# Kernel tuning notes

Measured on AMD Instinct MI355X. Metric: run time of the kernel, lower is better.

Reference implementation:

```python
import jax, jax.numpy as jnp
import numpy as np

T, K, F = 131072, 64, 8
EPS = 1e-10


def setup_inputs() -> dict:
    key = jax.random.key(0)
    k0, k1, k2, k3 = jax.random.split(key, 4)
    return {
        "observations": jax.random.normal(k0, (T, F), dtype=jnp.float32),
        "beta_logits": jax.random.normal(k1, (K,), dtype=jnp.float32),
        "pi_logits": jax.random.normal(k2, (K, K), dtype=jnp.float32),
        "means": 0.1 * jax.random.normal(k3, (K, F), dtype=jnp.float32),
        "log_vars": jnp.zeros((K, F), dtype=jnp.float32),
    }


def _stick_breaking(logits):
    betas = jax.nn.sigmoid(logits)
    cp = jnp.cumprod(1.0 - betas)
    return betas * jnp.concatenate([jnp.ones((1,), betas.dtype), cp[:-1]])


def _emission_log_probs(obs, means, log_vars):
    # Diagonal-covariance MVN log-prob, vectorized over (T, K) via matmuls
    # logN(x; mu, diag(v)) = -0.5 * (sum((x-mu)^2/v) + sum(log v) + F*log(2pi))
    inv_var = jnp.exp(-log_vars)                                 # (K, F)
    quad = (obs ** 2) @ inv_var.T                                # (T, K): sum x^2/v
    cross = obs @ (means * inv_var).T                            # (T, K): sum x*mu/v
    const = jnp.sum(means ** 2 * inv_var + log_vars, axis=1)     # (K,)
    log2pi = jnp.float32(np.log(2.0 * np.pi))
    Fdim = obs.shape[1]
    return -0.5 * (quad - 2.0 * cross + const[None, :] + Fdim * log2pi)


def reference(observations, beta_logits, pi_logits, means, log_vars):
    beta_w = _stick_breaking(beta_logits)                        # (K,)
    trans = jax.nn.softmax(pi_logits, axis=1)                    # (K, K)
    em = jnp.exp(_emission_log_probs(observations, means, log_vars))  # (T, K)

    # Forward recursion
    a0 = beta_w * em[0]
    a0 = a0 / (a0.sum() + EPS)

    def fwd_step(a, e):
        a = (a @ trans) * e
        a = a / (a.sum() + EPS)
        return a, a

    _, alpha_rest = jax.lax.scan(fwd_step, a0, em[1:])
    alpha = jnp.concatenate([a0[None, :], alpha_rest], axis=0)   # (T, K)

    # Backward recursion: beta[t] = normalize(trans @ (beta[t+1] * em[t+1]))
    bT = jnp.ones((trans.shape[0],), observations.dtype)

    def bwd_step(b, e_next):
        b = trans @ (b * e_next)
        b = b / (b.sum() + EPS)
        return b, b

    _, beta_rev = jax.lax.scan(bwd_step, bT, em[1:], reverse=True)
    beta = jnp.concatenate([beta_rev, bT[None, :]], axis=0)      # (T, K)

    log_likelihood = jnp.log(alpha[-1].sum() + EPS)
    return alpha, beta, log_likelihood
```

## Files before the change

### kernel.cpp

```cpp
#include <hip/hip_runtime.h>

#define T_N   131072
#define K_N   64
#define L_C   128
#define F_N   8
#define N_CH  (T_N / L_C)
#define WARM  96
#define EPS_F 1e-10f
#define OBS_MAX ((T_N - 1) * F_N)

#define LOG2E 1.4426950408889634f
#define NL2E  (-0.72134752044448170f)
#define LN2   0.6931471805599453f
#define LN2PI 1.8378770664093453f

typedef float v2f __attribute__((ext_vector_type(2)));

__device__ __forceinline__ float dpp_f(float x, const int ctrl) {
  return x;
}
#define DPPI(SRC, CTRL) __builtin_amdgcn_update_dpp(0, (SRC), (CTRL), 0xF, 0xF, true)
#define DPPF(SRC, CTRL) __int_as_float(DPPI(__float_as_int(SRC), (CTRL)))

template <int CTRL>
__device__ __forceinline__ float dpp_add(float x) {
  int y = __builtin_amdgcn_update_dpp(0, __float_as_int(x), CTRL, 0xF, 0xF, true);
  return x + __int_as_float(y);
}
__device__ __forceinline__ float wave_sum64(float x) {
  x = dpp_add<0x111>(x);
  x = dpp_add<0x112>(x);
  x = dpp_add<0x114>(x);
  x = dpp_add<0x118>(x);
  x = dpp_add<0x142>(x);
  x = dpp_add<0x143>(x);
  return __int_as_float(__builtin_amdgcn_readlane(__float_as_int(x), 63));
}

#define PKFMA(a, b, c) __builtin_elementwise_fma(a, b, c)

__device__ __forceinline__ float em_pk(const float4& xa, const float4& xb,
                                       const v2f civ2[4], const v2f cmiv2[4],
                                       float ccst) {
  v2f x0 = {xa.x, xa.y}, x1 = {xa.z, xa.w};
  v2f x2 = {xb.x, xb.y}, x3 = {xb.z, xb.w};
  v2f a0 = {ccst, 0.f}, a1 = {0.f, 0.f};
  a0 = PKFMA(x0, PKFMA(x0, civ2[0], cmiv2[0]), a0);
  a1 = PKFMA(x1, PKFMA(x1, civ2[1], cmiv2[1]), a1);
  a0 = PKFMA(x2, PKFMA(x2, civ2[2], cmiv2[2]), a0);
  a1 = PKFMA(x3, PKFMA(x3, civ2[3], cmiv2[3]), a1);
  v2f s = a0 + a1;
  return __builtin_amdgcn_exp2f(s.x + s.y);
}

#define MATVEC(VV, MOUT)                                                      \
  {                                                                           \
    float Gr[16];                                                             \
    Gr[0] = (VV);                                                             \
    Gr[1] = DPPF(Gr[0], 0xB1);                                 \
    Gr[2] = DPPF(Gr[0], 0x4E);                                 \
    Gr[3] = DPPF(Gr[1], 0x4E);                                                \
    _Pragma("unroll")                                                         \
    for (int rr = 0; rr < 4; ++rr) Gr[4 + rr] = DPPF(Gr[rr], 0x124);          \
    _Pragma("unroll")                                                         \
    for (int rr = 0; rr < 8; ++rr) Gr[8 + rr] = DPPF(Gr[rr], 0x128);          \
    v2f aE0 = {0.f,0.f}, aE1 = {0.f,0.f}, aO0 = {0.f,0.f}, aO1 = {0.f,0.f};   \
    _Pragma("unroll")                                                         \
    for (int rr = 0; rr < 8; ++rr) {                                          \
      v2f gg = {Gr[rr], Gr[rr]};                                              \
      aE0 = PKFMA(gg, TcE[rr], aE0);                                          \
      aO0 = PKFMA(gg, TcO[rr], aO0);                                          \
    }                                                                         \
    _Pragma("unroll")                                                         \
    for (int rr = 8; rr < 16; ++rr) {                                         \
      v2f gg = {Gr[rr], Gr[rr]};                                              \
      aE1 = PKFMA(gg, TcE[rr], aE1);                                          \
      aO1 = PKFMA(gg, TcO[rr], aO1);                                          \
    }                                                                         \
    v2f accE = aE0 + aE1, accO = aO0 + aO1;           \
    float kx = qb0 ? accO.x : accE.x, ky = qb0 ? accO.y : accE.y;             \
    float sx = qb0 ? accE.x : accO.x, sy = qb0 ? accE.y : accO.y;             \
    float rx = __int_as_float(                                                \
        __builtin_amdgcn_ds_swizzle(__float_as_int(sx), 0x401F));             \
    float ry = __int_as_float(                                                \
        __builtin_amdgcn_ds_swizzle(__float_as_int(sy), 0x401F));             \
    float c0 = kx + rx, c1 = ky + ry;                 \
    float keep2 = qb1 ? c1 : c0;                                              \
    float send2 = qb1 ? c0 : c1;                                              \
    float got = __int_as_float(                                               \
        __builtin_amdgcn_ds_bpermute(bpaddr, __float_as_int(send2)));         \
    MOUT = keep2 + got;                             \
  }

extern "C" __global__ void __launch_bounds__(64, 2)
hdphmm_fb(const float* __restrict__ obs,
          const float* __restrict__ beta_logits,
          const float* __restrict__ pi_logits,
          const float* __restrict__ means,
          const float* __restrict__ log_vars,
          float* __restrict__ out) {
  const int lane = threadIdx.x;
  const int bid  = blockIdx.x;
  const int h    = lane & 15;
  const int q    = lane >> 4;
  const bool qb0 = (q & 1);
  const bool qb1 = (q >> 1);
  const int bpaddr = (lane ^ 32) << 2;
  __shared__ __align__(8) float2 sstat[K_N];
  __shared__ float sb[K_N];

  float* alpha   = out;
  float* betaout = out + (size_t)T_N * K_N;

  v2f civ2[4], cmiv2[4];
  float ccst;
  {
    const float4* mp = reinterpret_cast<const float4*>(means + lane * F_N);
    const float4* lp = reinterpret_cast<const float4*>(log_vars + lane * F_N);
    float4 m0 = mp[0], m1 = mp[1];
    float4 l0 = lp[0], l1 = lp[1];
    float mu[8] = {m0.x, m0.y, m0.z, m0.w, m1.x, m1.y, m1.z, m1.w};
    float lv[8] = {l0.x, l0.y, l0.z, l0.w, l1.x, l1.y, l1.z, l1.w};
    float cst = F_N * LN2PI;
#pragma unroll
    for (int f = 0; f < 8; ++f) {
      float iv = __builtin_amdgcn_exp2f(-lv[f] * LOG2E);
      cst += lv[f] + mu[f] * mu[f] * iv;
      float cf  = NL2E * iv;
      civ2[f >> 1][f & 1]  = cf;
      cmiv2[f >> 1][f & 1] = -2.0f * mu[f] * cf;
    }
    ccst = NL2E * cst;
  }

  {
    const float4* pr4 = reinterpret_cast<const float4*>(pi_logits + lane * K_N);
    float mx = -3.0e38f;
#pragma unroll
    for (int k = 0; k < 16; ++k) {
      float4 r = pr4[k];
      mx = fmaxf(mx, fmaxf(fmaxf(r.x, r.y), fmaxf(r.z, r.w)));
    }
    float s = 0.0f;
#pragma unroll
    for (int k = 0; k < 16; ++k) {
      float4 r = pr4[k];
      s += __builtin_amdgcn_exp2f((r.x - mx) * LOG2E);
      s += __builtin_amdgcn_exp2f((r.y - mx) * LOG2E);
      s += __builtin_amdgcn_exp2f((r.z - mx) * LOG2E);
      s += __builtin_amdgcn_exp2f((r.w - mx) * LOG2E);
    }
    sstat[lane] = make_float2(mx, __builtin_amdgcn_rcpf(s));
  }
  __syncthreads();

  int ki[16];
  ki[0] = lane;
  ki[1] = DPPI(ki[0], 0xB1);
  ki[2] = DPPI(ki[0], 0x4E);
  ki[3] = DPPI(ki[1], 0x4E);
#pragma unroll
  for (int rr = 0; rr < 4; ++rr) ki[4 + rr] = DPPI(ki[rr], 0x124);
#pragma unroll
  for (int rr = 0; rr < 8; ++rr) ki[8 + rr] = DPPI(ki[rr], 0x128);

  if (bid < N_CH) {
    v2f TcE[16], TcO[16];
#pragma unroll
    for (int rr = 0; rr < 16; ++rr) {
      int k = ki[rr];
      float2 st = sstat[k];
      const float* pk = pi_logits + k * K_N;
      float e0 = __builtin_amdgcn_exp2f((pk[h]      - st.x) * LOG2E) * st.y;
      float e1 = __builtin_amdgcn_exp2f((pk[h + 16] - st.x) * LOG2E) * st.y;
      float e2 = __builtin_amdgcn_exp2f((pk[h + 32] - st.x) * LOG2E) * st.y;
      float e3 = __builtin_amdgcn_exp2f((pk[h + 48] - st.x) * LOG2E) * st.y;
      TcE[rr] = (v2f){e0, e2};
      TcO[rr] = (v2f){e1, e3};
    }

    const int out_lo = bid * L_C;
    float v;
    int t_first;
    if (bid == 0) {
      float bl = beta_logits[lane];
      float ex = __builtin_amdgcn_exp2f(-bl * LOG2E);
      float bw = __builtin_amdgcn_rcpf(1.0f + ex);
      sb[lane] = 1.0f - bw;
      __syncthreads();
      float pr = 1.0f;
#pragma unroll
      for (int i = 0; i < 64; ++i) {
        float qv = sb[i];
        pr = (i < lane) ? pr * qv : pr;
      }
      float4 x0 = reinterpret_cast<const float4*>(obs)[0];
      float4 x1 = reinterpret_cast<const float4*>(obs)[1];
      v = bw * pr * em_pk(x0, x1, civ2, cmiv2, ccst);
      t_first = 1;
    } else {
      const int t0 = out_lo - WARM;
      const float4* xp = reinterpret_cast<const float4*>(obs + t0 * F_N);
      v = em_pk(xp[0], xp[1], civ2, cmiv2, ccst);
      t_first = t0 + 1;
    }
    float S = wave_sum64(v);
    int obs_off = t_first * F_N;
    float4 xa, xb;
    {
      const float4* xp = reinterpret_cast<const float4*>(obs + obs_off);
      xa = xp[0]; xb = xp[1];
    }
    int out_off = out_lo * K_N + lane;

#define FWD_STEP(DO_STORE)                                                    \
  {                                                                           \
    int offn = obs_off + F_N; offn = (offn > OBS_MAX) ? OBS_MAX : offn;       \
    float4 nxa = *reinterpret_cast<const float4*>(obs + offn);                \
    float4 nxb = *reinterpret_cast<const float4*>(obs + offn + 4);            \
    float m;                                                                  \
    MATVEC(v, m)                                                              \
    float r = __builtin_amdgcn_rcpf(S + EPS_F);                               \
    if (DO_STORE) { alpha[out_off] = v * r; out_off += K_N; }                 \
    float e = em_pk(xa, xb, civ2, cmiv2, ccst);                               \
    float vn = m * r * e;                                                     \
    S = wave_sum64(vn);                                                       \
    v = vn; xa = nxa; xb = nxb; obs_off = offn;                               \
  }

    const int wn = (bid == 0) ? 0 : WARM;
#pragma unroll 1
    for (int it = 0; it < wn; ++it) FWD_STEP(0)
#pragma unroll 1
    for (int it = 0; it < L_C - 1; ++it) FWD_STEP(1)
#undef FWD_STEP
    float r = __builtin_amdgcn_rcpf(S + EPS_F);
    alpha[out_off] = v * r;
    if (bid == N_CH - 1 && lane == 0) {
      float sl = S * r + EPS_F;
      out[(size_t)2 * T_N * K_N] = __builtin_amdgcn_logf(sl) * LN2;
    }
  } else {
    v2f TcE[16], TcO[16];
    {
      float2 s0 = sstat[h], s1 = sstat[h + 16];
      float2 s2 = sstat[h + 32], s3 = sstat[h + 48];
#pragma unroll
      for (int rr = 0; rr < 16; ++rr) {
        int k = ki[rr];
        float p0 = pi_logits[h * K_N + k];
        float p1 = pi_logits[(h + 16) * K_N + k];
        float p2 = pi_logits[(h + 32) * K_N + k];
        float p3 = pi_logits[(h + 48) * K_N + k];
        TcE[rr] = (v2f){__builtin_amdgcn_exp2f((p0 - s0.x) * LOG2E) * s0.y,
                        __builtin_amdgcn_exp2f((p2 - s2.x) * LOG2E) * s2.y};
        TcO[rr] = (v2f){__builtin_amdgcn_exp2f((p1 - s1.x) * LOG2E) * s1.y,
                        __builtin_amdgcn_exp2f((p3 - s3.x) * LOG2E) * s3.y};
      }
    }
    const int cb   = bid - N_CH;
    const int t_lo = cb * L_C;
    const int t_hi = t_lo + L_C - 1;
    int t_top = t_hi + WARM;
    if (t_top > T_N - 1) t_top = T_N - 1;
    const int s_top = (cb == N_CH - 1) ? T_N - 2 : t_hi;

    float u = 1.0f, S = 1.0f;
    float w;
    {
      const float4* xp = reinterpret_cast<const float4*>(obs + t_top * F_N);
      w = em_pk(xp[0], xp[1], civ2, cmiv2, ccst);
    }
    if (cb == N_CH - 1)
      betaout[(size_t)(T_N - 1) * K_N + lane] = 1.0f;
    int obs_off = (t_top - 1) * F_N;
    float4 xa, xb;
    {
      const float4* xp = reinterpret_cast<const float4*>(obs + obs_off);
      xa = xp[0]; xb = xp[1];
    }
    int out_off = s_top * K_N + lane;

#define BWD_STEP(DO_STORE)                                                    \
  {                                                                           \
    int offn = obs_off - F_N; offn = (offn < 0) ? 0 : offn;                   \
    float4 nxa = *reinterpret_cast<const float4*>(obs + offn);                \
    float4 nxb = *reinterpret_cast<const float4*>(obs + offn + 4);            \
    float m;                                                                  \
    MATVEC(w, m)                                                              \
    float r = __builtin_amdgcn_rcpf(S + EPS_F);                               \
    if (DO_STORE) { betaout[out_off] = u * r; out_off -= K_N; }               \
    float u2 = m * r;                                                         \
    float e = em_pk(xa, xb, civ2, cmiv2, ccst);                               \
    w = u2 * e;                                                               \
    S = wave_sum64(u2);                                                       \
    u = u2; xa = nxa; xb = nxb; obs_off = offn;                               \
  }

    const int warm_n  = t_top - s_top;
    const int store_n = s_top - t_lo;
#pragma unroll 1
    for (int it = 0; it < warm_n; ++it) BWD_STEP(0)
#pragma unroll 1
    for (int it = 0; it < store_n; ++it) BWD_STEP(1)
#undef BWD_STEP
    betaout[t_lo * K_N + lane] = u * __builtin_amdgcn_rcpf(S + EPS_F);
  }
}

extern "C" void kernel_launch(void* const* d_in, const int* in_sizes, int n_in,
                              void* d_out, int out_size, void* d_ws, size_t ws_size,
                              hipStream_t stream) {
  (void)in_sizes; (void)n_in; (void)out_size; (void)d_ws; (void)ws_size;
  const float* obs  = (const float*)d_in[0];
  const float* bl   = (const float*)d_in[1];
  const float* pi   = (const float*)d_in[2];
  const float* mns  = (const float*)d_in[3];
  const float* lvs  = (const float*)d_in[4];
  hipLaunchKernelGGL(hdphmm_fb, dim3(2 * N_CH), dim3(64), 0, stream,
                     obs, bl, pi, mns, lvs, (float*)d_out);
}
```

Before: 181.2 us.

## Batch warm-up normalisation every eight steps and use permlane swaps in matvec

During the warm-up phase of both the forward and backward chunked recursions, the per-step wave reduction and reciprocal are replaced by a renormalisation every eight steps. Emissions are scaled by a constant exponent offset so values stay in range between renormalisations. The matvec cross-quadrant reduction now uses permlane16/32 swap builtins where available, replacing ds_swizzle and ds_bpermute. The storing loops compute the reciprocal one step ahead and are unrolled by two. The intent is to shorten the serial critical path per step, at the cost of more reliance on the fixed scale offset to avoid overflow or underflow.

```diff
diff --git a/kernel.cpp b/kernel.cpp
--- a/kernel.cpp
+++ b/kernel.cpp
@@ -13,12 +13,11 @@
 #define NL2E  (-0.72134752044448170f)
 #define LN2   0.6931471805599453f
 #define LN2PI 1.8378770664093453f
+#define EMSC  16.0f
 
 typedef float v2f __attribute__((ext_vector_type(2)));
-
-__device__ __forceinline__ float dpp_f(float x, const int ctrl) {
-  return x;
-}
+typedef unsigned uint2v __attribute__((ext_vector_type(2)));
+
 #define DPPI(SRC, CTRL) __builtin_amdgcn_update_dpp(0, (SRC), (CTRL), 0xF, 0xF, true)
 #define DPPF(SRC, CTRL) __int_as_float(DPPI(__float_as_int(SRC), (CTRL)))
 
@@ -37,14 +36,38 @@
   return __int_as_float(__builtin_amdgcn_readlane(__float_as_int(x), 63));
 }
 
+#if __has_builtin(__builtin_amdgcn_permlane16_swap) && \
+    __has_builtin(__builtin_amdgcn_permlane32_swap)
+__device__ __forceinline__ float psum16(float x) {
+  uint2v r = __builtin_amdgcn_permlane16_swap(__float_as_uint(x),
+                                              __float_as_uint(x), false, false);
+  return __uint_as_float(r.x) + __uint_as_float(r.y);
+}
+__device__ __forceinline__ float psum32(float x) {
+  uint2v r = __builtin_amdgcn_permlane32_swap(__float_as_uint(x),
+                                              __float_as_uint(x), false, false);
+  return __uint_as_float(r.x) + __uint_as_float(r.y);
+}
+#else
+__device__ __forceinline__ float psum16(float x) {
+  return x + __int_as_float(
+      __builtin_amdgcn_ds_swizzle(__float_as_int(x), 0x401F));
+}
+__device__ __forceinline__ float psum32(float x) {
+  int addr = (((int)threadIdx.x ^ 32) & 63) << 2;
+  return x + __int_as_float(
+      __builtin_amdgcn_ds_bpermute(addr, __float_as_int(x)));
+}
+#endif
+
 #define PKFMA(a, b, c) __builtin_elementwise_fma(a, b, c)
 
 __device__ __forceinline__ float em_pk(const float4& xa, const float4& xb,
                                        const v2f civ2[4], const v2f cmiv2[4],
-                                       float ccst) {
+                                       float cc) {
   v2f x0 = {xa.x, xa.y}, x1 = {xa.z, xa.w};
   v2f x2 = {xb.x, xb.y}, x3 = {xb.z, xb.w};
-  v2f a0 = {ccst, 0.f}, a1 = {0.f, 0.f};
+  v2f a0 = {cc, 0.f}, a1 = {0.f, 0.f};
   a0 = PKFMA(x0, PKFMA(x0, civ2[0], cmiv2[0]), a0);
   a1 = PKFMA(x1, PKFMA(x1, civ2[1], cmiv2[1]), a1);
   a0 = PKFMA(x2, PKFMA(x2, civ2[2], cmiv2[2]), a0);
@@ -78,18 +101,13 @@
       aO1 = PKFMA(gg, TcO[rr], aO1);                                          \
     }                                                                         \
     v2f accE = aE0 + aE1, accO = aO0 + aO1;           \
-    float kx = qb0 ? accO.x : accE.x, ky = qb0 ? accO.y : accE.y;             \
-    float sx = qb0 ? accE.x : accO.x, sy = qb0 ? accE.y : accO.y;             \
-    float rx = __int_as_float(                                                \
-        __builtin_amdgcn_ds_swizzle(__float_as_int(sx), 0x401F));             \
-    float ry = __int_as_float(                                                \
-        __builtin_amdgcn_ds_swizzle(__float_as_int(sy), 0x401F));             \
-    float c0 = kx + rx, c1 = ky + ry;                 \
-    float keep2 = qb1 ? c1 : c0;                                              \
-    float send2 = qb1 ? c0 : c1;                                              \
-    float got = __int_as_float(                                               \
-        __builtin_amdgcn_ds_bpermute(bpaddr, __float_as_int(send2)));         \
-    MOUT = keep2 + got;                             \
+    float pe0 = psum32(accE.x), pe2 = psum32(accE.y);                         \
+    float po1 = psum32(accO.x), po3 = psum32(accO.y);                         \
+    pe0 = psum16(pe0); pe2 = psum16(pe2);                                     \
+    po1 = psum16(po1); po3 = psum16(po3);                                     \
+    float tE = qb1 ? pe2 : pe0;                                               \
+    float tO = qb1 ? po3 : po1;                                               \
+    MOUT = qb0 ? tO : tE;                                                     \
   }
 
 extern "C" __global__ void __launch_bounds__(64, 2)
@@ -102,10 +120,8 @@
   const int lane = threadIdx.x;
   const int bid  = blockIdx.x;
   const int h    = lane & 15;
-  const int q    = lane >> 4;
-  const bool qb0 = (q & 1);
-  const bool qb1 = (q >> 1);
-  const int bpaddr = (lane ^ 32) << 2;
+  const bool qb0 = (lane >> 4) & 1;
+  const bool qb1 = (lane >> 5) & 1;
   __shared__ __align__(8) float2 sstat[K_N];
   __shared__ float sb[K_N];
 
@@ -113,7 +129,7 @@
   float* betaout = out + (size_t)T_N * K_N;
 
   v2f civ2[4], cmiv2[4];
-  float ccst;
+  float c0, cw;
   {
     const float4* mp = reinterpret_cast<const float4*>(means + lane * F_N);
     const float4* lp = reinterpret_cast<const float4*>(log_vars + lane * F_N);
@@ -130,7 +146,8 @@
       civ2[f >> 1][f & 1]  = cf;
       cmiv2[f >> 1][f & 1] = -2.0f * mu[f] * cf;
     }
-    ccst = NL2E * cst;
+    c0 = NL2E * cst;
+    cw = c0 + EMSC;
   }
 
   {
@@ -196,15 +213,14 @@
       }
       float4 x0 = reinterpret_cast<const float4*>(obs)[0];
       float4 x1 = reinterpret_cast<const float4*>(obs)[1];
-      v = bw * pr * em_pk(x0, x1, civ2, cmiv2, ccst);
+      v = bw * pr * em_pk(x0, x1, civ2, cmiv2, c0);
       t_first = 1;
     } else {
       const int t0 = out_lo - WARM;
       const float4* xp = reinterpret_cast<const float4*>(obs + t0 * F_N);
-      v = em_pk(xp[0], xp[1], civ2, cmiv2, ccst);
+      v = em_pk(xp[0], xp[1], civ2, cmiv2, cw);
       t_first = t0 + 1;
     }
-    float S = wave_sum64(v);
     int obs_off = t_first * F_N;
     float4 xa, xb;
     {
@@ -213,31 +229,47 @@
     }
     int out_off = out_lo * K_N + lane;
 
-#define FWD_STEP(DO_STORE)                                                    \
+    const int wn8 = (bid == 0) ? 0 : (WARM >> 3);
+#pragma unroll 1
+    for (int o = 0; o < wn8; ++o) {
+#pragma unroll
+      for (int i = 0; i < 8; ++i) {
+        float4 nxa = *reinterpret_cast<const float4*>(obs + obs_off + F_N);
+        float4 nxb = *reinterpret_cast<const float4*>(obs + obs_off + F_N + 4);
+        float m;
+        MATVEC(v, m)
+        float e = em_pk(xa, xb, civ2, cmiv2, cw);
+        v = m * e;
+        xa = nxa; xb = nxb; obs_off += F_N;
+      }
+      float Sw = wave_sum64(v);
+      v *= __builtin_amdgcn_rcpf(Sw);
+    }
+
+    float S = wave_sum64(v);
+    float r_st = __builtin_amdgcn_rcpf(S + EPS_F);
+
+#define FWD_SSTEP                                                             \
   {                                                                           \
     int offn = obs_off + F_N; offn = (offn > OBS_MAX) ? OBS_MAX : offn;       \
     float4 nxa = *reinterpret_cast<const float4*>(obs + offn);                \
     float4 nxb = *reinterpret_cast<const float4*>(obs + offn + 4);            \
     float m;                                                                  \
     MATVEC(v, m)                                                              \
-    float r = __builtin_amdgcn_rcpf(S + EPS_F);                               \
-    if (DO_STORE) { alpha[out_off] = v * r; out_off += K_N; }                 \
-    float e = em_pk(xa, xb, civ2, cmiv2, ccst);                               \
-    float vn = m * r * e;                                                     \
+    alpha[out_off] = v * r_st; out_off += K_N;                                \
+    float e = em_pk(xa, xb, civ2, cmiv2, c0);                                 \
+    float vn = m * (r_st * e);                                                \
     S = wave_sum64(vn);                                                       \
+    r_st = __builtin_amdgcn_rcpf(S + EPS_F);                                  \
     v = vn; xa = nxa; xb = nxb; obs_off = offn;                               \
   }
 
-    const int wn = (bid == 0) ? 0 : WARM;
-#pragma unroll 1
-    for (int it = 0; it < wn; ++it) FWD_STEP(0)
-#pragma unroll 1
-    for (int it = 0; it < L_C - 1; ++it) FWD_STEP(1)
-#undef FWD_STEP
-    float r = __builtin_amdgcn_rcpf(S + EPS_F);
-    alpha[out_off] = v * r;
+#pragma unroll 2
+    for (int it = 0; it < L_C - 1; ++it) FWD_SSTEP
+#undef FWD_SSTEP
+    alpha[out_off] = v * r_st;
     if (bid == N_CH - 1 && lane == 0) {
-      float sl = S * r + EPS_F;
+      float sl = S * r_st + EPS_F;
       out[(size_t)2 * T_N * K_N] = __builtin_amdgcn_logf(sl) * LN2;
     }
   } else {
@@ -265,11 +297,10 @@
     if (t_top > T_N - 1) t_top = T_N - 1;
     const int s_top = (cb == N_CH - 1) ? T_N - 2 : t_hi;
 
-    float u = 1.0f, S = 1.0f;
     float w;
     {
       const float4* xp = reinterpret_cast<const float4*>(obs + t_top * F_N);
-      w = em_pk(xp[0], xp[1], civ2, cmiv2, ccst);
+      w = em_pk(xp[0], xp[1], civ2, cmiv2, cw);
     }
     if (cb == N_CH - 1)
       betaout[(size_t)(T_N - 1) * K_N + lane] = 1.0f;
@@ -281,30 +312,67 @@
     }
     int out_off = s_top * K_N + lane;
 
-#define BWD_STEP(DO_STORE)                                                    \
+#define BWD_WSTEP                                                             \
+  {                                                                           \
+    float4 nxa = *reinterpret_cast<const float4*>(obs + obs_off - F_N);       \
+    float4 nxb = *reinterpret_cast<const float4*>(obs + obs_off - F_N + 4);   \
+    float m;                                                                  \
+    MATVEC(w, m)                                                              \
+    float e = em_pk(xa, xb, civ2, cmiv2, cw);                                 \
+    w = m * e;                                                                \
+    xa = nxa; xb = nxb; obs_off -= F_N;                                       \
+  }
+
+    const int pw  = (t_top - s_top) - 1;
+    const int pw8 = pw >> 3, pwr = pw & 7;
+#pragma unroll 1
+    for (int o = 0; o < pw8; ++o) {
+#pragma unroll
+      for (int i = 0; i < 8; ++i) BWD_WSTEP
+      float Sw = wave_sum64(w);
+      w *= __builtin_amdgcn_rcpf(Sw);
+    }
+#pragma unroll 1
+    for (int it = 0; it < pwr; ++it) BWD_WSTEP
+#undef BWD_WSTEP
+
+    float u, S, r_st;
+    {
+      float m;
+      MATVEC(w, m)
+      float Sm = wave_sum64(m);
+      u = m * __builtin_amdgcn_rcpf(Sm);
+      float e = em_pk(xa, xb, civ2, cmiv2, c0);
+      w = u * e;
+      S = wave_sum64(u);
+      r_st = __builtin_amdgcn_rcpf(S + EPS_F);
+      int offn = obs_off - F_N; offn = (offn < 0) ? 0 : offn;
+      xa = *reinterpret_cast<const float4*>(obs + offn);
+      xb = *reinterpret_cast<const float4*>(obs + offn + 4);
+      obs_off = offn;
+    }
+
+#define BWD_SSTEP                                                             \
   {                                                                           \
     int offn = obs_off - F_N; offn = (offn < 0) ? 0 : offn;                   \
     float4 nxa = *reinterpret_cast<const float4*>(obs + offn);                \
     float4 nxb = *reinterpret_cast<const float4*>(obs + offn + 4);            \
     float m;                                                                  \
     MATVEC(w, m)                                                              \
-    float r = __builtin_amdgcn_rcpf(S + EPS_F);                               \
-    if (DO_STORE) { betaout[out_off] = u * r; out_off -= K_N; }               \
-    float u2 = m * r;                                                         \
-    float e = em_pk(xa, xb, civ2, cmiv2, ccst);                               \
+    betaout[out_off] = u * r_st; out_off -= K_N;                              \
+    float u2 = m * r_st;                                                      \
+    float e = em_pk(xa, xb, civ2, cmiv2, c0);                                 \
     w = u2 * e;                                                               \
     S = wave_sum64(u2);                                                       \
+    r_st = __builtin_amdgcn_rcpf(S + EPS_F);                                  \
     u = u2; xa = nxa; xb = nxb; obs_off = offn;                               \
   }
 
-    const int warm_n  = t_top - s_top;
     const int store_n = s_top - t_lo;
-#pragma unroll 1
-    for (int it = 0; it < warm_n; ++it) BWD_STEP(0)
-#pragma unroll 1
-    for (int it = 0; it < store_n; ++it) BWD_STEP(1)
-#undef BWD_STEP
-    betaout[t_lo * K_N + lane] = u * __builtin_amdgcn_rcpf(S + EPS_F);
+#pragma unroll 2
+    for (int it = 0; it < store_n; ++it) BWD_SSTEP
+#undef BWD_SSTEP
+    betaout[t_lo * K_N + lane] = u * r_st;
   }
 }
 
```

After: 181.0 us. Within noise of the previous version (-0.1%).
